# Performance work log

Measured on AMD Instinct MI355X. Metric: run time of the kernel, lower is better.

Reference implementation:

```python
import jax, jax.numpy as jnp
import numpy as np

B, S, D, H = 4, 2048, 1024, 16
HD = D // H  # head size = 64


def setup_inputs() -> dict:
    key = jax.random.key(0)
    ks = jax.random.split(key, 9)
    scale = 1.0 / np.sqrt(D)
    x = jax.random.normal(ks[0], (B, S, D), dtype=jnp.float32)
    Wq = jax.random.normal(ks[1], (D, D), dtype=jnp.float32) * scale
    Wk = jax.random.normal(ks[2], (D, D), dtype=jnp.float32) * scale
    Wv = jax.random.normal(ks[3], (D, D), dtype=jnp.float32) * scale
    Wo = jax.random.normal(ks[4], (D, D), dtype=jnp.float32) * scale
    bq = jax.random.normal(ks[5], (D,), dtype=jnp.float32) * 0.01
    bk = jax.random.normal(ks[6], (D,), dtype=jnp.float32) * 0.01
    bv = jax.random.normal(ks[7], (D,), dtype=jnp.float32) * 0.01
    bo = jax.random.normal(ks[8], (D,), dtype=jnp.float32) * 0.01
    return {"x": x, "Wq": Wq, "bq": bq, "Wk": Wk, "bk": bk,
            "Wv": Wv, "bv": bv, "Wo": Wo, "bo": bo}


def reference(x, Wq, bq, Wk, bk, Wv, bv, Wo, bo):
    Bv, Sv, Dv = x.shape
    # QKV projections (torch Linear: x @ W^T + b; here W stored as [in, out])
    q = x @ Wq + bq  # [B,S,D]
    k = x @ Wk + bk
    v = x @ Wv + bv
    # split heads -> [B,H,S,HD]
    q = q.reshape(Bv, Sv, H, HD).transpose(0, 2, 1, 3)
    k = k.reshape(Bv, Sv, H, HD).transpose(0, 2, 1, 3)
    v = v.reshape(Bv, Sv, H, HD).transpose(0, 2, 1, 3)
    # scaled scores + additive causal mask (upper triangle -> -inf)
    scores = jnp.einsum('bhqd,bhkd->bhqk', q, k) * (1.0 / np.sqrt(HD))
    causal = jnp.triu(jnp.full((Sv, Sv), -jnp.inf, dtype=scores.dtype), k=1)
    attn = jax.nn.softmax(scores + causal, axis=-1)
    # dropout is identity in eval / p=0
    out = jnp.einsum('bhqk,bhkd->bhqd', attn, v)
    out = out.transpose(0, 2, 1, 3).reshape(Bv, Sv, Dv)
    return out @ Wo + bo
```

## Files before the change

### kernel.cpp

```cpp
#include <hip/hip_runtime.h>
#include <hip/hip_bf16.h>


typedef unsigned short u16;
typedef short bf16x8 __attribute__((ext_vector_type(8)));
typedef float f32x4 __attribute__((ext_vector_type(4)));

constexpr int NB = 4, NS = 2048, ND = 1024, NH = 16, NHD = 64;
constexpr int NM = NB * NS;
constexpr float NEG = -1e30f;
constexpr int PAD = 68;
constexpr int EPAD = 136;

__device__ __forceinline__ u16 f2bf(float f) {
  union { float f; unsigned int u; } c; c.f = f;
  unsigned int r = (c.u + 0x7FFFu + ((c.u >> 16) & 1u)) >> 16;
  return (u16)r;
}
__device__ __forceinline__ unsigned int pk2bf(float a, float b) {
  float2 t; t.x = a; t.y = b;
  __hip_bfloat162 h = __float22bfloat162_rn(t);
  unsigned int u; __builtin_memcpy(&u, &h, 4); return u;
}
__device__ __forceinline__ void g2lds16(const u16* g, u16* l) {
  __builtin_amdgcn_global_load_lds(
      (const __attribute__((address_space(1))) void*)g,
      (__attribute__((address_space(3))) void*)l, 16, 0, 0);
}
__device__ __forceinline__ bf16x8 ldsw(const u16* b, int row, int cq) {
  return *(const bf16x8*)&b[row * 64 + ((cq ^ (row & 7)) << 3)];
}

__global__ __launch_bounds__(256) void fill_kernel(float* __restrict__ p, float v, int n) {
  int i = blockIdx.x * 256 + threadIdx.x;
  if (i < n) p[i] = v;
}

__global__ __launch_bounds__(256) void cvt_kernel(const float* __restrict__ in,
                                                  u16* __restrict__ out, int n4) {
  int i = blockIdx.x * 256 + threadIdx.x;
  if (i < n4) {
    float4 f = ((const float4*)in)[i];
    ushort4 o;
    o.x = f2bf(f.x); o.y = f2bf(f.y); o.z = f2bf(f.z); o.w = f2bf(f.w);
    ((ushort4*)out)[i] = o;
  }
}

__global__ __launch_bounds__(256) void wt_kernel(
    const float* __restrict__ s0, const float* __restrict__ s1,
    const float* __restrict__ s2, const float* __restrict__ s3,
    u16* __restrict__ d0, u16* __restrict__ d1,
    u16* __restrict__ d2, u16* __restrict__ d3) {
  const int z = blockIdx.z;
  const float* S = (z == 0) ? s0 : (z == 1) ? s1 : (z == 2) ? s2 : s3;
  u16* D = (z == 0) ? d0 : (z == 1) ? d1 : (z == 2) ? d2 : d3;
  __shared__ u16 t[64][68];
  const int r0 = blockIdx.x * 64, c0 = blockIdx.y * 64;
  const int tid = threadIdx.x;
#pragma unroll
  for (int i = 0; i < 4; i++) {
    int row = (tid >> 4) + i * 16;
    int col = (tid & 15) * 4;
    float4 f = *(const float4*)&S[(long)(r0 + row) * ND + c0 + col];
    ushort4 u; u.x = f2bf(f.x); u.y = f2bf(f.y); u.z = f2bf(f.z); u.w = f2bf(f.w);
    *(ushort4*)&t[row][col] = u;
  }
  __syncthreads();
#pragma unroll
  for (int i = 0; i < 4; i++) {
    int nrow = (tid >> 4) + i * 16;
    int kcol = (tid & 15) * 4;
    ushort4 u;
    u.x = t[kcol + 0][nrow]; u.y = t[kcol + 1][nrow];
    u.z = t[kcol + 2][nrow]; u.w = t[kcol + 3][nrow];
    *(ushort4*)&D[(long)(c0 + nrow) * ND + r0 + kcol] = u;
  }
}

__global__ __launch_bounds__(256, 3) void gemm_qkv_kernel(
    const float* __restrict__ Xf, const u16* __restrict__ Xb,
    const u16* __restrict__ WtQ,
    const float* __restrict__ bqp, const float* __restrict__ bkp,
    const float* __restrict__ bvp,
    u16* __restrict__ Qw, u16* __restrict__ Kw, u16* __restrict__ Vtw,
    int xmode) {
  __shared__ __attribute__((aligned(16))) u16 SMEM[128 * EPAD];
  u16* Asm = SMEM;
  u16* Bsm = SMEM + 8192;
  const int m0 = blockIdx.x * 128;
  const int ng = blockIdx.y;
  const int mat = ng >> 3, n0 = (ng & 7) * 128;
  const u16* Wt = WtQ + (long)mat * ND * ND;
  const int tid = threadIdx.x;
  const int w = tid >> 6, lane = tid & 63, quad = lane >> 4, lr = lane & 15;
  const int wm = w & 1, wn = w >> 1;
  const int b_r = lane >> 3, b_c = lane & 7;

  f32x4 acc[4][4] = {};

  for (int k0 = 0; k0 < ND; k0 += 64) {
    __syncthreads();
    if (xmode == 0) {
#pragma unroll
      for (int j = 0; j < 4; j++) {
        int r = w * 32 + j * 8 + b_r;
        const float* src = Xf + (long)(m0 + r) * ND + k0 + ((b_c ^ (r & 7)) << 3);
        float4 f0 = *(const float4*)src;
        float4 f1 = *(const float4*)(src + 4);
        uint4 d;
        d.x = pk2bf(f0.x, f0.y); d.y = pk2bf(f0.z, f0.w);
        d.z = pk2bf(f1.x, f1.y); d.w = pk2bf(f1.z, f1.w);
        *(uint4*)&Asm[r * 64 + (b_c << 3)] = d;
      }
    } else {
#pragma unroll
      for (int j = 0; j < 4; j++) {
        int R0 = w * 32 + j * 8;
        int r = R0 + b_r;
        g2lds16(Xb + (long)(m0 + r) * ND + k0 + ((b_c ^ (r & 7)) << 3),
                &Asm[R0 * 64]);
      }
    }
#pragma unroll
    for (int j = 0; j < 4; j++) {
      int R0 = w * 32 + j * 8;
      int r = R0 + b_r;
      g2lds16(Wt + (long)(n0 + r) * ND + k0 + ((b_c ^ (r & 7)) << 3),
              &Bsm[R0 * 64]);
    }
    __syncthreads();

#pragma unroll
    for (int kk = 0; kk < 2; kk++) {
      bf16x8 af[4], bfr[4];
#pragma unroll
      for (int mt = 0; mt < 4; mt++)
        af[mt] = ldsw(Asm, wm * 64 + mt * 16 + lr, kk * 4 + quad);
#pragma unroll
      for (int nt = 0; nt < 4; nt++)
        bfr[nt] = ldsw(Bsm, wn * 64 + nt * 16 + lr, kk * 4 + quad);
#pragma unroll
      for (int nt = 0; nt < 4; nt++)
#pragma unroll
        for (int mt = 0; mt < 4; mt++)
          acc[nt][mt] = __builtin_amdgcn_mfma_f32_16x16x32_bf16(
              af[mt], bfr[nt], acc[nt][mt], 0, 0, 0);
    }
  }

  const float* bias = (mat == 0) ? bqp : (mat == 1) ? bkp : bvp;
  __syncthreads();
  if (mat < 2) {
#pragma unroll
    for (int nt = 0; nt < 4; nt++) {
      int n_loc = wn * 64 + nt * 16 + lr;
      float bn = bias[n0 + n_loc];
#pragma unroll
      for (int mt = 0; mt < 4; mt++)
#pragma unroll
        for (int r = 0; r < 4; r++) {
          int m_loc = wm * 64 + mt * 16 + quad * 4 + r;
          SMEM[m_loc * EPAD + n_loc] = f2bf(acc[nt][mt][r] + bn);
        }
    }
    __syncthreads();
    u16* Yv = (mat == 0) ? Qw : Kw;
#pragma unroll
    for (int pass = 0; pass < 8; pass++) {
      int row = pass * 16 + (tid >> 4), c = tid & 15;
      uint4 d = *(const uint4*)&SMEM[row * EPAD + c * 8];
      int n_g = n0 + c * 8, h_ = n_g >> 6, hd_ = n_g & (NHD - 1);
      int m = m0 + row, b_ = m >> 11, s_ = m & (NS - 1);
      *(uint4*)&Yv[((long)((b_ * NH + h_) * NS + s_)) * NHD + hd_] = d;
    }
  } else {
#pragma unroll
    for (int nt = 0; nt < 4; nt++) {
      int n_loc = wn * 64 + nt * 16 + lr;
      float bn = bias[n0 + n_loc];
#pragma unroll
      for (int mt = 0; mt < 4; mt++) {
        int m_base = wm * 64 + mt * 16 + quad * 4;
        uint2 d;
        d.x = pk2bf(acc[nt][mt][0] + bn, acc[nt][mt][1] + bn);
        d.y = pk2bf(acc[nt][mt][2] + bn, acc[nt][mt][3] + bn);
        *(uint2*)&SMEM[n_loc * EPAD + m_base] = d;
      }
    }
    __syncthreads();
#pragma unroll
    for (int pass = 0; pass < 8; pass++) {
      int plane = pass * 16 + (tid >> 4), mc = tid & 15;
      uint4 d = *(const uint4*)&SMEM[plane * EPAD + mc * 8];
      int n_g = n0 + plane, h_ = n_g >> 6, hd_ = n_g & (NHD - 1);
      int m = m0 + mc * 8, b_ = m >> 11, s_ = m & (NS - 1);
      *(uint4*)&Vtw[((long)((b_ * NH + h_) * NHD + hd_)) * NS + s_] = d;
    }
  }
}

__global__ __launch_bounds__(256, 3) void gemm_out_kernel(
    const u16* __restrict__ Xg, const u16* __restrict__ Wt,
    const float* __restrict__ bias, float* __restrict__ Y) {
  __shared__ __attribute__((aligned(16))) u16 Asm[128 * 64];
  __shared__ __attribute__((aligned(16))) u16 Bsm[128 * 64];
  const int m0 = blockIdx.x * 128, n0 = blockIdx.y * 128;
  const int tid = threadIdx.x;
  const int w = tid >> 6, lane = tid & 63, quad = lane >> 4, lr = lane & 15;
  const int wm = w & 1, wn = w >> 1;
  const int b_r = lane >> 3, b_c = lane & 7;

  f32x4 acc[4][4] = {};

  for (int k0 = 0; k0 < ND; k0 += 64) {
    __syncthreads();
    const int h_ = k0 >> 6;
#pragma unroll
    for (int j = 0; j < 4; j++) {
      int R0 = w * 32 + j * 8;
      int r = R0 + b_r;
      int mrow = m0 + r, b_ = mrow >> 11, s_ = mrow & (NS - 1);
      g2lds16(Xg + ((long)((b_ * NH + h_) * NS + s_)) * NHD + ((b_c ^ (r & 7)) << 3),
              &Asm[R0 * 64]);
      g2lds16(Wt + (long)(n0 + r) * ND + k0 + ((b_c ^ (r & 7)) << 3),
              &Bsm[R0 * 64]);
    }
    __syncthreads();

#pragma unroll
    for (int kk = 0; kk < 2; kk++) {
      bf16x8 af[4], bfr[4];
#pragma unroll
      for (int mt = 0; mt < 4; mt++)
        af[mt] = ldsw(Asm, wm * 64 + mt * 16 + lr, kk * 4 + quad);
#pragma unroll
      for (int nt = 0; nt < 4; nt++)
        bfr[nt] = ldsw(Bsm, wn * 64 + nt * 16 + lr, kk * 4 + quad);
#pragma unroll
      for (int nt = 0; nt < 4; nt++)
#pragma unroll
        for (int mt = 0; mt < 4; mt++)
          acc[nt][mt] = __builtin_amdgcn_mfma_f32_16x16x32_bf16(
              af[mt], bfr[nt], acc[nt][mt], 0, 0, 0);
    }
  }

#pragma unroll
  for (int nt = 0; nt < 4; nt++) {
    int n = n0 + wn * 64 + nt * 16 + lr;
    float bn = bias[n];
#pragma unroll
    for (int mt = 0; mt < 4; mt++) {
#pragma unroll
      for (int r = 0; r < 4; r++) {
        int m = m0 + wm * 64 + mt * 16 + quad * 4 + r;
        Y[(long)m * ND + n] = acc[nt][mt][r] + bn;
      }
    }
  }
}

__global__ __launch_bounds__(512) void attn_kernel(
    u16* __restrict__ Q, const u16* __restrict__ K, const u16* __restrict__ Vtg) {
  __shared__ __attribute__((aligned(16))) u16 Klds[64 * PAD];
  __shared__ __attribute__((aligned(16))) u16 Vt[64 * PAD];
  __shared__ __attribute__((aligned(16))) u16 Pbuf[8][16 * PAD];
  const int bh = blockIdx.x;
  const int qt = 15 - blockIdx.y;
  const int q0 = qt * 128;
  const int tid = threadIdx.x;
  const int w = tid >> 6, lane = tid & 63, quad = lane >> 4, lr = lane & 15;
  u16* Qb = Q + (long)bh * NS * NHD;
  const u16* Kb = K + (long)bh * NS * NHD;
  const u16* Vb = Vtg + (long)bh * NHD * NS;

  const int qw0 = q0 + w * 16;
  bf16x8 qf[2];
  {
    int m = qw0 + lr;
    qf[0] = *(const bf16x8*)&Qb[(long)m * NHD + quad * 8];
    qf[1] = *(const bf16x8*)&Qb[(long)m * NHD + 32 + quad * 8];
  }
  const bf16x8 ones = {0x3F80, 0x3F80, 0x3F80, 0x3F80,
                       0x3F80, 0x3F80, 0x3F80, 0x3F80};

  f32x4 oacc[4] = {};
  f32x4 lacc = {};

  const int srow = tid >> 3, sc8 = (tid & 7) * 8;
  const float kexp = 0.125f * 1.4426950408889634f;
  const int jmax = q0 + 64;

  for (int j0 = 0; j0 <= jmax; j0 += 64) {
    __syncthreads();
    *(uint4*)&Klds[srow * PAD + sc8] =
        *(const uint4*)&Kb[(long)(j0 + srow) * NHD + sc8];
    *(uint4*)&Vt[srow * PAD + sc8] =
        *(const uint4*)&Vb[(long)srow * NS + j0 + sc8];
    __syncthreads();

    if (j0 > qw0 + 15) continue;

    f32x4 sc[4] = {};
#pragma unroll
    for (int t = 0; t < 4; t++) {
      bf16x8 kf0 = *(bf16x8*)&Klds[(t * 16 + lr) * PAD + quad * 8];
      bf16x8 kf1 = *(bf16x8*)&Klds[(t * 16 + lr) * PAD + 32 + quad * 8];
      sc[t] = __builtin_amdgcn_mfma_f32_16x16x32_bf16(qf[0], kf0, sc[t], 0, 0, 0);
      sc[t] = __builtin_amdgcn_mfma_f32_16x16x32_bf16(qf[1], kf1, sc[t], 0, 0, 0);
    }

    if (j0 + 63 > qw0) {
#pragma unroll
      for (int t = 0; t < 4; t++)
#pragma unroll
        for (int r = 0; r < 4; r++)
          if ((j0 + t * 16 + lr) > (qw0 + quad * 4 + r)) sc[t][r] = NEG;
    }

#pragma unroll
    for (int t = 0; t < 4; t++) {
#pragma unroll
      for (int r = 0; r < 4; r++) sc[t][r] = exp2f(sc[t][r] * kexp);
      unsigned int p01 = pk2bf(sc[t][0], sc[t][1]);
      unsigned int p23 = pk2bf(sc[t][2], sc[t][3]);
      int col = t * 16 + lr;
      Pbuf[w][(quad * 4 + 0) * PAD + col] = (u16)p01;
      Pbuf[w][(quad * 4 + 1) * PAD + col] = (u16)(p01 >> 16);
      Pbuf[w][(quad * 4 + 2) * PAD + col] = (u16)p23;
      Pbuf[w][(quad * 4 + 3) * PAD + col] = (u16)(p23 >> 16);
    }

    bf16x8 pf0 = *(bf16x8*)&Pbuf[w][lr * PAD + quad * 8];
    bf16x8 pf1 = *(bf16x8*)&Pbuf[w][lr * PAD + 32 + quad * 8];
    lacc = __builtin_amdgcn_mfma_f32_16x16x32_bf16(pf0, ones, lacc, 0, 0, 0);
    lacc = __builtin_amdgcn_mfma_f32_16x16x32_bf16(pf1, ones, lacc, 0, 0, 0);
#pragma unroll
    for (int t = 0; t < 4; t++) {
      bf16x8 vf0 = *(bf16x8*)&Vt[(t * 16 + lr) * PAD + quad * 8];
      bf16x8 vf1 = *(bf16x8*)&Vt[(t * 16 + lr) * PAD + 32 + quad * 8];
      oacc[t] = __builtin_amdgcn_mfma_f32_16x16x32_bf16(pf0, vf0, oacc[t], 0, 0, 0);
      oacc[t] = __builtin_amdgcn_mfma_f32_16x16x32_bf16(pf1, vf1, oacc[t], 0, 0, 0);
    }
  }

  float inv[4];
#pragma unroll
  for (int r = 0; r < 4; r++) inv[r] = 1.0f / lacc[r];
#pragma unroll
  for (int t = 0; t < 4; t++) {
#pragma unroll
    for (int r = 0; r < 4; r++) {
      int qg = qw0 + quad * 4 + r;
      int hd_ = t * 16 + lr;
      Qb[(long)qg * NHD + hd_] = f2bf(oacc[t][r] * inv[r]);
    }
  }
}

extern "C" void kernel_launch(void* const* d_in, const int* in_sizes, int n_in,
                              void* d_out, int out_size, void* d_ws, size_t ws_size,
                              hipStream_t stream) {
  const float* x  = (const float*)d_in[0];
  const float* Wq = (const float*)d_in[1];
  const float* bq = (const float*)d_in[2];
  const float* Wk = (const float*)d_in[3];
  const float* bk = (const float*)d_in[4];
  const float* Wv = (const float*)d_in[5];
  const float* bv = (const float*)d_in[6];
  const float* Wo = (const float*)d_in[7];
  const float* bo = (const float*)d_in[8];

  const size_t BUF = (size_t)NM * ND * sizeof(u16);
  if (ws_size < 2 * BUF) {
    fill_kernel<<<(out_size + 255) / 256, 256, 0, stream>>>((float*)d_out, 0.f, out_size);
    return;
  }

  u16* Qw  = (u16*)d_ws;
  u16* Vtw = Qw + (long)NM * ND;
  u16* Kw  = (u16*)d_out;
  u16* WtQ = Kw + (long)NM * ND;
  u16* WtO = WtQ + 3L * ND * ND;
  const bool bigws = ws_size >= 3 * BUF;
  u16* Xb = bigws ? (Vtw + (long)NM * ND) : nullptr;

  wt_kernel<<<dim3(16, 16, 4), 256, 0, stream>>>(Wq, Wk, Wv, Wo,
      WtQ, WtQ + (long)ND * ND, WtQ + 2L * ND * ND, WtO);
  if (bigws)
    cvt_kernel<<<(NM * ND / 4 + 255) / 256, 256, 0, stream>>>(x, Xb, NM * ND / 4);

  gemm_qkv_kernel<<<dim3(64, 24), 256, 0, stream>>>(
      x, Xb, WtQ, bq, bk, bv, Qw, Kw, Vtw, bigws ? 2 : 0);
  attn_kernel<<<dim3(NB * NH, NS / 128), 512, 0, stream>>>(Qw, Kw, Vtw);
  hipMemcpyAsync(Vtw, WtO, (size_t)ND * ND * sizeof(u16),
                 hipMemcpyDeviceToDevice, stream);
  gemm_out_kernel<<<dim3(64, 8), 256, 0, stream>>>(Qw, Vtw, bo, (float*)d_out);
}
```

Before: 266.3 us.

## Compute transposed scores so P stays in registers, drop LDS P buffer

The attention kernel now computes S^T (K as the A operand, Q as B), so each lane already holds probabilities in the layout the PV MFMA needs as its B operand. The per-warp LDS round trip for P (scalar u16 stores plus re-reads) is removed. To keep the MFMA k-dimension consistent, V^T columns are permuted when staged into LDS. The output is accumulated transposed and written as packed 8-byte stores. The cost is a more intricate V staging pattern with two 8-byte LDS stores per thread instead of one 16-byte store.

```diff
diff --git a/kernel.cpp b/kernel.cpp
--- a/kernel.cpp
+++ b/kernel.cpp
@@ -265,7 +265,6 @@
     u16* __restrict__ Q, const u16* __restrict__ K, const u16* __restrict__ Vtg) {
   __shared__ __attribute__((aligned(16))) u16 Klds[64 * PAD];
   __shared__ __attribute__((aligned(16))) u16 Vt[64 * PAD];
-  __shared__ __attribute__((aligned(16))) u16 Pbuf[8][16 * PAD];
   const int bh = blockIdx.x;
   const int qt = 15 - blockIdx.y;
   const int q0 = qt * 128;
@@ -285,30 +284,36 @@
   const bf16x8 ones = {0x3F80, 0x3F80, 0x3F80, 0x3F80,
                        0x3F80, 0x3F80, 0x3F80, 0x3F80};
 
-  f32x4 oacc[4] = {};
+  f32x4 oaccT[4] = {};
   f32x4 lacc = {};
 
-  const int srow = tid >> 3, sc8 = (tid & 7) * 8;
+  const int srow = tid >> 3, sa = tid & 7;
+  const int vcb = (sa >> 2) * 32 + ((sa & 1) << 4) + (((sa >> 1) & 1) << 2);
   const float kexp = 0.125f * 1.4426950408889634f;
   const int jmax = q0 + 64;
 
   for (int j0 = 0; j0 <= jmax; j0 += 64) {
     __syncthreads();
-    *(uint4*)&Klds[srow * PAD + sc8] =
-        *(const uint4*)&Kb[(long)(j0 + srow) * NHD + sc8];
-    *(uint4*)&Vt[srow * PAD + sc8] =
-        *(const uint4*)&Vb[(long)srow * NS + j0 + sc8];
+    *(uint4*)&Klds[srow * PAD + sa * 8] =
+        *(const uint4*)&Kb[(long)(j0 + srow) * NHD + sa * 8];
+    {
+      uint4 v = *(const uint4*)&Vb[(long)srow * NS + j0 + sa * 8];
+      uint2 v01; v01.x = v.x; v01.y = v.y;
+      uint2 v23; v23.x = v.z; v23.y = v.w;
+      *(uint2*)&Vt[srow * PAD + vcb] = v01;
+      *(uint2*)&Vt[srow * PAD + vcb + 8] = v23;
+    }
     __syncthreads();
 
     if (j0 > qw0 + 15) continue;
 
-    f32x4 sc[4] = {};
+    f32x4 scT[4] = {};
 #pragma unroll
     for (int t = 0; t < 4; t++) {
       bf16x8 kf0 = *(bf16x8*)&Klds[(t * 16 + lr) * PAD + quad * 8];
       bf16x8 kf1 = *(bf16x8*)&Klds[(t * 16 + lr) * PAD + 32 + quad * 8];
-      sc[t] = __builtin_amdgcn_mfma_f32_16x16x32_bf16(qf[0], kf0, sc[t], 0, 0, 0);
-      sc[t] = __builtin_amdgcn_mfma_f32_16x16x32_bf16(qf[1], kf1, sc[t], 0, 0, 0);
+      scT[t] = __builtin_amdgcn_mfma_f32_16x16x32_bf16(kf0, qf[0], scT[t], 0, 0, 0);
+      scT[t] = __builtin_amdgcn_mfma_f32_16x16x32_bf16(kf1, qf[1], scT[t], 0, 0, 0);
     }
 
     if (j0 + 63 > qw0) {
@@ -316,46 +321,38 @@
       for (int t = 0; t < 4; t++)
 #pragma unroll
         for (int r = 0; r < 4; r++)
-          if ((j0 + t * 16 + lr) > (qw0 + quad * 4 + r)) sc[t][r] = NEG;
-    }
-
-#pragma unroll
-    for (int t = 0; t < 4; t++) {
-#pragma unroll
-      for (int r = 0; r < 4; r++) sc[t][r] = exp2f(sc[t][r] * kexp);
-      unsigned int p01 = pk2bf(sc[t][0], sc[t][1]);
-      unsigned int p23 = pk2bf(sc[t][2], sc[t][3]);
-      int col = t * 16 + lr;
-      Pbuf[w][(quad * 4 + 0) * PAD + col] = (u16)p01;
-      Pbuf[w][(quad * 4 + 1) * PAD + col] = (u16)(p01 >> 16);
-      Pbuf[w][(quad * 4 + 2) * PAD + col] = (u16)p23;
-      Pbuf[w][(quad * 4 + 3) * PAD + col] = (u16)(p23 >> 16);
-    }
-
-    bf16x8 pf0 = *(bf16x8*)&Pbuf[w][lr * PAD + quad * 8];
-    bf16x8 pf1 = *(bf16x8*)&Pbuf[w][lr * PAD + 32 + quad * 8];
-    lacc = __builtin_amdgcn_mfma_f32_16x16x32_bf16(pf0, ones, lacc, 0, 0, 0);
-    lacc = __builtin_amdgcn_mfma_f32_16x16x32_bf16(pf1, ones, lacc, 0, 0, 0);
-#pragma unroll
-    for (int t = 0; t < 4; t++) {
-      bf16x8 vf0 = *(bf16x8*)&Vt[(t * 16 + lr) * PAD + quad * 8];
-      bf16x8 vf1 = *(bf16x8*)&Vt[(t * 16 + lr) * PAD + 32 + quad * 8];
-      oacc[t] = __builtin_amdgcn_mfma_f32_16x16x32_bf16(pf0, vf0, oacc[t], 0, 0, 0);
-      oacc[t] = __builtin_amdgcn_mfma_f32_16x16x32_bf16(pf1, vf1, oacc[t], 0, 0, 0);
-    }
-  }
-
-  float inv[4];
-#pragma unroll
-  for (int r = 0; r < 4; r++) inv[r] = 1.0f / lacc[r];
-#pragma unroll
-  for (int t = 0; t < 4; t++) {
-#pragma unroll
-    for (int r = 0; r < 4; r++) {
-      int qg = qw0 + quad * 4 + r;
-      int hd_ = t * 16 + lr;
-      Qb[(long)qg * NHD + hd_] = f2bf(oacc[t][r] * inv[r]);
-    }
+          if ((j0 + t * 16 + quad * 4 + r) > (qw0 + lr)) scT[t][r] = NEG;
+    }
+
+#pragma unroll
+    for (int t = 0; t < 4; t++)
+#pragma unroll
+      for (int r = 0; r < 4; r++) scT[t][r] = exp2f(scT[t][r] * kexp);
+
+#pragma unroll
+    for (int kk = 0; kk < 2; kk++) {
+      uint4 pu;
+      pu.x = pk2bf(scT[2 * kk][0], scT[2 * kk][1]);
+      pu.y = pk2bf(scT[2 * kk][2], scT[2 * kk][3]);
+      pu.z = pk2bf(scT[2 * kk + 1][0], scT[2 * kk + 1][1]);
+      pu.w = pk2bf(scT[2 * kk + 1][2], scT[2 * kk + 1][3]);
+      bf16x8 pt; __builtin_memcpy(&pt, &pu, 16);
+      lacc = __builtin_amdgcn_mfma_f32_16x16x32_bf16(ones, pt, lacc, 0, 0, 0);
+#pragma unroll
+      for (int dt = 0; dt < 4; dt++) {
+        bf16x8 va = *(bf16x8*)&Vt[(dt * 16 + lr) * PAD + kk * 32 + quad * 8];
+        oaccT[dt] = __builtin_amdgcn_mfma_f32_16x16x32_bf16(va, pt, oaccT[dt], 0, 0, 0);
+      }
+    }
+  }
+
+  const float inv = 1.0f / lacc[0];
+#pragma unroll
+  for (int dt = 0; dt < 4; dt++) {
+    uint2 o;
+    o.x = pk2bf(oaccT[dt][0] * inv, oaccT[dt][1] * inv);
+    o.y = pk2bf(oaccT[dt][2] * inv, oaccT[dt][3] * inv);
+    *(uint2*)&Qb[(long)(qw0 + lr) * NHD + dt * 16 + quad * 4] = o;
   }
 }
 
```

After: 244.3 us. 1.09x faster.
